# Optimization experiments

Measured on AMD Instinct MI355X. Metric: run time of the kernel, lower is better.

The kernel has to match this reference:

```python
import jax, jax.numpy as jnp
import numpy as np

WIN = (8, 8)
NUM_HEADS = 8
DIM = 256


def _relative_position_index(wh, ww):
    ch = np.arange(wh)
    cw = np.arange(ww)
    coords = np.stack(np.meshgrid(ch, cw, indexing='ij'))  # [2, wh, ww]
    cf = coords.reshape(2, -1)                              # [2, N]
    rel = cf[:, :, None] - cf[:, None, :]                   # [2, N, N]
    rel = rel.transpose(1, 2, 0).copy()
    rel[:, :, 0] += wh - 1
    rel[:, :, 1] += ww - 1
    rel[:, :, 0] *= 2 * ww - 1
    return rel.sum(-1).astype(np.int32)                     # [N, N]


def setup_inputs() -> dict:
    key = jax.random.key(0)
    ks = jax.random.split(key, 7)
    N = WIN[0] * WIN[1]
    BW = 4096  # num_windows * batch
    x = jax.random.normal(ks[0], (BW, N, DIM), dtype=jnp.float32)
    # 0 / -inf style shift mask; random 0 or -100 per entry for generality
    mask = jnp.where(jax.random.uniform(ks[1], (BW, N, N)) < 0.2, -100.0, 0.0).astype(jnp.float32)
    rpb_table = jax.random.normal(ks[2], ((2 * WIN[0] - 1) * (2 * WIN[1] - 1), NUM_HEADS), dtype=jnp.float32) * 0.02
    qkv_w = jax.random.normal(ks[3], (3 * DIM, DIM), dtype=jnp.float32) * (DIM ** -0.5)
    qkv_b = jax.random.normal(ks[4], (3 * DIM,), dtype=jnp.float32) * 0.01
    proj_w = jax.random.normal(ks[5], (DIM, DIM), dtype=jnp.float32) * (DIM ** -0.5)
    proj_b = jax.random.normal(ks[6], (DIM,), dtype=jnp.float32) * 0.01
    rel_idx = jnp.asarray(_relative_position_index(*WIN))
    return {"x": x, "mask": mask, "rpb_table": rpb_table, "qkv_w": qkv_w,
            "qkv_b": qkv_b, "proj_w": proj_w, "proj_b": proj_b, "rel_idx": rel_idx}


def reference(x, mask, rpb_table, qkv_w, qkv_b, proj_w, proj_b, rel_idx):
    B_, N, C = x.shape
    H = NUM_HEADS
    hd = C // H
    scale = hd ** -0.5
    qkv = x @ qkv_w.T + qkv_b                               # [B_, N, 3C]
    qkv = qkv.reshape(B_, N, 3, H, hd).transpose(2, 0, 3, 1, 4)  # [3, B_, H, N, hd]
    q, k, v = qkv[0], qkv[1], qkv[2]
    attn = jnp.einsum('bhnd,bhmd->bhnm', q * scale, k)      # [B_, H, N, N]
    bias = rpb_table[rel_idx.reshape(-1)].reshape(N, N, H).transpose(2, 0, 1)  # [H, N, N]
    attn = attn + bias[None]
    nW = mask.shape[0]
    attn = attn.reshape(B_ // nW, nW, H, N, N) + mask[None, :, None]
    attn = attn.reshape(B_, H, N, N)
    attn = jax.nn.softmax(attn, axis=-1)
    out = jnp.einsum('bhnm,bhmd->bhnd', attn, v)            # [B_, H, N, hd]
    out = out.transpose(0, 2, 1, 3).reshape(B_, N, C)
    return out @ proj_w.T + proj_b
```

## Files before the change

### kernel.cpp

```cpp
#include <hip/hip_runtime.h>

typedef _Float16 half_t;
typedef __attribute__((ext_vector_type(4))) _Float16 half4;
typedef __attribute__((ext_vector_type(8))) _Float16 half8;
typedef __attribute__((ext_vector_type(4))) float f32x4;

#define WS_W1   0
#define WS_W2   (768*256*2)
#define WS_BIAS (WS_W2 + 256*256*2)
#define QK_SCALE 0.17677669529663687f

__global__ __launch_bounds__(256) void prep_kernel(
    const float* __restrict__ qkv_w, const float* __restrict__ proj_w,
    const float* __restrict__ rpb, const int* __restrict__ rel_idx,
    char* __restrict__ ws) {
  int tid = blockIdx.x * 256 + threadIdx.x;
  half_t* W1 = (half_t*)(ws + WS_W1);
  half_t* W2 = (half_t*)(ws + WS_W2);
  float* BIASP = (float*)(ws + WS_BIAS);
  if (tid < 768 * 256) {
    int n = tid >> 8;
    float v = qkv_w[tid];
    if (n < 256) v *= QK_SCALE;
    W1[tid] = (half_t)v;
  }
  if (tid < 256 * 256) W2[tid] = (half_t)proj_w[tid];
  if (tid < 8 * 4096) {
    int r   = tid & 3;
    int l16 = (tid >> 2) & 15;
    int q   = (tid >> 6) & 3;
    int nt  = (tid >> 8) & 3;
    int mt  = (tid >> 10) & 3;
    int h   = (tid >> 12) & 7;
    int i = 16 * mt + l16;
    int j = 16 * nt + 4 * q + r;
    BIASP[tid] = rpb[rel_idx[i * 64 + j] * 8 + h];
  }
}

__device__ __forceinline__ void qkv_gemm(const half_t* Xs, const half_t* W1,
                                         int n0, int l16, int quad,
                                         f32x4 acc[2][4]) {
#pragma unroll
  for (int ks = 0; ks < 8; ++ks) {
    half8 af[4];
#pragma unroll
    for (int mt = 0; mt < 4; ++mt)
      af[mt] = *(const half8*)(&Xs[(16 * mt + l16) * 264 + 32 * ks + quad * 8]);
#pragma unroll
    for (int nt = 0; nt < 2; ++nt) {
      half8 bf = *(const half8*)(&W1[(size_t)(n0 + 16 * nt + l16) * 256 + 32 * ks + quad * 8]);
#pragma unroll
      for (int mt = 0; mt < 4; ++mt)
        acc[nt][mt] = __builtin_amdgcn_mfma_f32_16x16x32_f16(af[mt], bf, acc[nt][mt], 0, 0, 0);
    }
  }
}

__global__ __attribute__((amdgpu_flat_work_group_size(512, 512),
                          amdgpu_waves_per_eu(4, 4))) void fused_kernel(
    const float* __restrict__ x, const float* __restrict__ mask,
    const float* __restrict__ qkv_b, const float* __restrict__ proj_b,
    const char* __restrict__ ws, float* __restrict__ out, int nW) {
  __shared__ __align__(16) half_t Xs[64 * 264];
  __shared__ __align__(16) half_t Ms[64 * 68];
  __shared__ __align__(16) half_t Scr[8][2304];

  const int b = blockIdx.x;
  const int tid = threadIdx.x;
  const int wave = tid >> 6, lane = tid & 63;
  const int l16 = lane & 15, quad = lane >> 4;
  const f32x4 z4 = {0.f, 0.f, 0.f, 0.f};
  const half_t* W1 = (const half_t*)(ws + WS_W1);
  half_t* Sw = &Scr[wave][0];

  {
    const float4* xw = (const float4*)(x + (size_t)b * 16384);
#pragma unroll
    for (int i = 0; i < 8; ++i) {
      int idx4 = tid + i * 512;
      float4 v = xw[idx4];
      int e = idx4 << 2;
      int row = e >> 8, col = e & 255;
      half4 pk;
      pk[0] = (half_t)v.x; pk[1] = (half_t)v.y; pk[2] = (half_t)v.z; pk[3] = (half_t)v.w;
      *(half4*)(&Xs[row * 264 + col]) = pk;
    }
    const float4* mw = (const float4*)(mask + (size_t)(b % nW) * 4096);
#pragma unroll
    for (int i = 0; i < 2; ++i) {
      int idx4 = tid + i * 512;
      float4 v = mw[idx4];
      int e = idx4 << 2;
      int mi = e >> 6, mj = e & 63;
      half4 pk;
      pk[0] = (half_t)v.x; pk[1] = (half_t)v.y; pk[2] = (half_t)v.z; pk[3] = (half_t)v.w;
      *(half4*)(&Ms[mi * 68 + mj]) = pk;
    }
  }
  __syncthreads();

  const int h = wave;
  half4 vh[2][4];
  half8 qf[4];
  half8 kf[4];

  {
    f32x4 acc[2][4];
#pragma unroll
    for (int nt = 0; nt < 2; ++nt)
#pragma unroll
      for (int mt = 0; mt < 4; ++mt) acc[nt][mt] = z4;
    const int n0 = 512 + 32 * h;
    qkv_gemm(Xs, W1, n0, l16, quad, acc);
#pragma unroll
    for (int nt = 0; nt < 2; ++nt) {
      float vb = qkv_b[n0 + 16 * nt + l16];
#pragma unroll
      for (int mt = 0; mt < 4; ++mt)
#pragma unroll
        for (int r = 0; r < 4; ++r)
          vh[nt][mt][r] = (half_t)(acc[nt][mt][r] + vb);
    }
  }

  {
    f32x4 acc[2][4];
#pragma unroll
    for (int nt = 0; nt < 2; ++nt)
#pragma unroll
      for (int mt = 0; mt < 4; ++mt) acc[nt][mt] = z4;
    const int n0 = 32 * h;
    qkv_gemm(Xs, W1, n0, l16, quad, acc);
#pragma unroll
    for (int nt = 0; nt < 2; ++nt) {
      float qb = qkv_b[n0 + 16 * nt + l16] * QK_SCALE;
#pragma unroll
      for (int mt = 0; mt < 4; ++mt)
#pragma unroll
        for (int r = 0; r < 4; ++r)
          Sw[(16 * mt + 4 * quad + r) * 36 + 16 * nt + l16] = (half_t)(acc[nt][mt][r] + qb);
    }
#pragma unroll
    for (int mt = 0; mt < 4; ++mt) {
      union { half8 v; half4 hh[2]; } u;
      u.hh[0] = *(const half4*)(&Sw[(16 * mt + l16) * 36 + quad * 8]);
      u.hh[1] = *(const half4*)(&Sw[(16 * mt + l16) * 36 + quad * 8 + 4]);
      qf[mt] = u.v;
    }
    asm volatile("s_waitcnt lgkmcnt(0)" ::: "memory");
  }

  {
    f32x4 acc[2][4];
#pragma unroll
    for (int nt = 0; nt < 2; ++nt)
#pragma unroll
      for (int mt = 0; mt < 4; ++mt) acc[nt][mt] = z4;
    const int n0 = 256 + 32 * h;
    qkv_gemm(Xs, W1, n0, l16, quad, acc);
#pragma unroll
    for (int nt = 0; nt < 2; ++nt) {
      float kb = qkv_b[n0 + 16 * nt + l16];
#pragma unroll
      for (int mt = 0; mt < 4; ++mt)
#pragma unroll
        for (int r = 0; r < 4; ++r)
          Sw[(16 * mt + 4 * quad + r) * 36 + 16 * nt + l16] = (half_t)(acc[nt][mt][r] + kb);
    }
#pragma unroll
    for (int jt = 0; jt < 4; ++jt) {
      union { half8 v; half4 hh[2]; } u;
      u.hh[0] = *(const half4*)(&Sw[(16 * jt + l16) * 36 + quad * 8]);
      u.hh[1] = *(const half4*)(&Sw[(16 * jt + l16) * 36 + quad * 8 + 4]);
      kf[jt] = u.v;
    }
  }

  half4 oh[4][2];
  {
    const float4* BP4 = (const float4*)(ws + WS_BIAS);
#pragma unroll
    for (int it = 0; it < 4; ++it) {
      f32x4 Sj[4];
#pragma unroll
      for (int jt = 0; jt < 4; ++jt)
        Sj[jt] = __builtin_amdgcn_mfma_f32_16x16x32_f16(kf[jt], qf[it], z4, 0, 0, 0);
#pragma unroll
      for (int jt = 0; jt < 4; ++jt) {
        float4 bv = BP4[(size_t)(((h * 4 + it) * 4 + jt) * 64) + quad * 16 + l16];
        half4 mk = *(const half4*)(&Ms[(16 * it + l16) * 68 + 16 * jt + 4 * quad]);
#pragma unroll
        for (int r = 0; r < 4; ++r)
          Sj[jt][r] += ((const float*)&bv)[r] + (float)mk[r];
      }
      float mx = Sj[0][0];
#pragma unroll
      for (int jt = 0; jt < 4; ++jt)
#pragma unroll
        for (int r = 0; r < 4; ++r) mx = fmaxf(mx, Sj[jt][r]);
      mx = fmaxf(mx, __shfl_xor(mx, 16, 64));
      mx = fmaxf(mx, __shfl_xor(mx, 32, 64));
      float s = 0.f;
      half4 ph[4];
#pragma unroll
      for (int jt = 0; jt < 4; ++jt)
#pragma unroll
        for (int r = 0; r < 4; ++r) {
          float e = exp2f((Sj[jt][r] - mx) * 1.44269504f);
          s += e;
          ph[jt][r] = (half_t)e;
        }
      s += __shfl_xor(s, 16, 64);
      s += __shfl_xor(s, 32, 64);
      float linv = __builtin_amdgcn_rcpf(s);
      f32x4 o0 = z4, o1 = z4;
#pragma unroll
      for (int jt = 0; jt < 4; ++jt) {
        o0 = __builtin_amdgcn_mfma_f32_16x16x16f16(vh[0][jt], ph[jt], o0, 0, 0, 0);
        o1 = __builtin_amdgcn_mfma_f32_16x16x16f16(vh[1][jt], ph[jt], o1, 0, 0, 0);
      }
#pragma unroll
      for (int r = 0; r < 4; ++r) {
        oh[it][0][r] = (half_t)(o0[r] * linv);
        oh[it][1][r] = (half_t)(o1[r] * linv);
      }
    }
  }
  __syncthreads();

#pragma unroll
  for (int it = 0; it < 4; ++it)
#pragma unroll
    for (int dt = 0; dt < 2; ++dt)
      *(half4*)(&Xs[(16 * it + l16) * 264 + 32 * h + 16 * dt + 4 * quad]) = oh[it][dt];
  __syncthreads();

  {
    const half_t* W2 = (const half_t*)(ws + WS_W2);
    const int nb = wave * 32;
    f32x4 C[2][4];
#pragma unroll
    for (int nt = 0; nt < 2; ++nt)
#pragma unroll
      for (int mt = 0; mt < 4; ++mt) C[nt][mt] = z4;
#pragma unroll
    for (int ks = 0; ks < 8; ++ks) {
      half8 af[4];
#pragma unroll
      for (int mt = 0; mt < 4; ++mt)
        af[mt] = *(const half8*)(&Xs[(16 * mt + l16) * 264 + 32 * ks + quad * 8]);
#pragma unroll
      for (int nt = 0; nt < 2; ++nt) {
        half8 bf = *(const half8*)(&W2[(size_t)(nb + 16 * nt + l16) * 256 + 32 * ks + quad * 8]);
#pragma unroll
        for (int mt = 0; mt < 4; ++mt)
          C[nt][mt] = __builtin_amdgcn_mfma_f32_16x16x32_f16(af[mt], bf, C[nt][mt], 0, 0, 0);
      }
    }
#pragma unroll
    for (int nt = 0; nt < 2; ++nt) {
      int c = nb + 16 * nt + l16;
      float pb = proj_b[c];
#pragma unroll
      for (int mt = 0; mt < 4; ++mt)
#pragma unroll
        for (int r = 0; r < 4; ++r) {
          int t = 16 * mt + 4 * quad + r;
          out[(size_t)b * 16384 + t * 256 + c] = C[nt][mt][r] + pb;
        }
    }
  }
}

extern "C" void kernel_launch(void* const* d_in, const int* in_sizes, int n_in,
                              void* d_out, int out_size, void* d_ws, size_t ws_size,
                              hipStream_t stream) {
  const float* x      = (const float*)d_in[0];
  const float* mask   = (const float*)d_in[1];
  const float* rpb    = (const float*)d_in[2];
  const float* qkv_w  = (const float*)d_in[3];
  const float* qkv_b  = (const float*)d_in[4];
  const float* proj_w = (const float*)d_in[5];
  const float* proj_b = (const float*)d_in[6];
  const int*   rel    = (const int*)d_in[7];
  float* out = (float*)d_out;
  char* ws = (char*)d_ws;
  int B_ = in_sizes[0] / 16384;
  int nW = in_sizes[1] / 4096;
  hipLaunchKernelGGL(prep_kernel, dim3(768), dim3(256), 0, stream,
                     qkv_w, proj_w, rpb, rel, ws);
  hipLaunchKernelGGL(fused_kernel, dim3(B_), dim3(512), 0, stream,
                     x, mask, qkv_b, proj_b, (const char*)ws, out, nW);
}
```

Before: 829.2 us.

## Halve block to 4 waves handling two heads each, read mask from global

The fused kernel now launches 256 threads per window instead of 512. Each wave handles two attention heads in sequence and computes 64 output columns in the projection GEMM. The mask is no longer staged in LDS as fp16; it is read directly from global memory as float4 inside the softmax loop, and the scratch area shrinks to four waves. The aim is to cut LDS use so more blocks fit per CU and to drop the mask staging pass. The cost is less parallelism per block, more serial work per wave, higher register pressure from the doubled accumulators, and scattered global mask loads.

```diff
diff --git a/kernel.cpp b/kernel.cpp
--- a/kernel.cpp
+++ b/kernel.cpp
@@ -57,14 +57,13 @@
   }
 }
 
-__global__ __attribute__((amdgpu_flat_work_group_size(512, 512),
-                          amdgpu_waves_per_eu(4, 4))) void fused_kernel(
+__global__ __attribute__((amdgpu_flat_work_group_size(256, 256),
+                          amdgpu_waves_per_eu(3, 3))) void fused_kernel(
     const float* __restrict__ x, const float* __restrict__ mask,
     const float* __restrict__ qkv_b, const float* __restrict__ proj_b,
     const char* __restrict__ ws, float* __restrict__ out, int nW) {
   __shared__ __align__(16) half_t Xs[64 * 264];
-  __shared__ __align__(16) half_t Ms[64 * 68];
-  __shared__ __align__(16) half_t Scr[8][2304];
+  __shared__ __align__(16) half_t Scr[4][2304];
 
   const int b = blockIdx.x;
   const int tid = threadIdx.x;
@@ -77,8 +76,8 @@
   {
     const float4* xw = (const float4*)(x + (size_t)b * 16384);
 #pragma unroll
-    for (int i = 0; i < 8; ++i) {
-      int idx4 = tid + i * 512;
+    for (int i = 0; i < 16; ++i) {
+      int idx4 = tid + i * 256;
       float4 v = xw[idx4];
       int e = idx4 << 2;
       int row = e >> 8, col = e & 255;
@@ -86,100 +85,93 @@
       pk[0] = (half_t)v.x; pk[1] = (half_t)v.y; pk[2] = (half_t)v.z; pk[3] = (half_t)v.w;
       *(half4*)(&Xs[row * 264 + col]) = pk;
     }
-    const float4* mw = (const float4*)(mask + (size_t)(b % nW) * 4096);
-#pragma unroll
-    for (int i = 0; i < 2; ++i) {
-      int idx4 = tid + i * 512;
-      float4 v = mw[idx4];
-      int e = idx4 << 2;
-      int mi = e >> 6, mj = e & 63;
-      half4 pk;
-      pk[0] = (half_t)v.x; pk[1] = (half_t)v.y; pk[2] = (half_t)v.z; pk[3] = (half_t)v.w;
-      *(half4*)(&Ms[mi * 68 + mj]) = pk;
-    }
   }
   __syncthreads();
 
-  const int h = wave;
-  half4 vh[2][4];
-  half8 qf[4];
-  half8 kf[4];
-
-  {
-    f32x4 acc[2][4];
-#pragma unroll
-    for (int nt = 0; nt < 2; ++nt)
-#pragma unroll
-      for (int mt = 0; mt < 4; ++mt) acc[nt][mt] = z4;
-    const int n0 = 512 + 32 * h;
-    qkv_gemm(Xs, W1, n0, l16, quad, acc);
-#pragma unroll
-    for (int nt = 0; nt < 2; ++nt) {
-      float vb = qkv_b[n0 + 16 * nt + l16];
-#pragma unroll
-      for (int mt = 0; mt < 4; ++mt)
-#pragma unroll
-        for (int r = 0; r < 4; ++r)
-          vh[nt][mt][r] = (half_t)(acc[nt][mt][r] + vb);
-    }
-  }
-
-  {
-    f32x4 acc[2][4];
-#pragma unroll
-    for (int nt = 0; nt < 2; ++nt)
-#pragma unroll
-      for (int mt = 0; mt < 4; ++mt) acc[nt][mt] = z4;
-    const int n0 = 32 * h;
-    qkv_gemm(Xs, W1, n0, l16, quad, acc);
-#pragma unroll
-    for (int nt = 0; nt < 2; ++nt) {
-      float qb = qkv_b[n0 + 16 * nt + l16] * QK_SCALE;
-#pragma unroll
-      for (int mt = 0; mt < 4; ++mt)
-#pragma unroll
-        for (int r = 0; r < 4; ++r)
-          Sw[(16 * mt + 4 * quad + r) * 36 + 16 * nt + l16] = (half_t)(acc[nt][mt][r] + qb);
-    }
-#pragma unroll
-    for (int mt = 0; mt < 4; ++mt) {
-      union { half8 v; half4 hh[2]; } u;
-      u.hh[0] = *(const half4*)(&Sw[(16 * mt + l16) * 36 + quad * 8]);
-      u.hh[1] = *(const half4*)(&Sw[(16 * mt + l16) * 36 + quad * 8 + 4]);
-      qf[mt] = u.v;
-    }
-    asm volatile("s_waitcnt lgkmcnt(0)" ::: "memory");
-  }
-
-  {
-    f32x4 acc[2][4];
-#pragma unroll
-    for (int nt = 0; nt < 2; ++nt)
-#pragma unroll
-      for (int mt = 0; mt < 4; ++mt) acc[nt][mt] = z4;
-    const int n0 = 256 + 32 * h;
-    qkv_gemm(Xs, W1, n0, l16, quad, acc);
-#pragma unroll
-    for (int nt = 0; nt < 2; ++nt) {
-      float kb = qkv_b[n0 + 16 * nt + l16];
-#pragma unroll
-      for (int mt = 0; mt < 4; ++mt)
-#pragma unroll
-        for (int r = 0; r < 4; ++r)
-          Sw[(16 * mt + 4 * quad + r) * 36 + 16 * nt + l16] = (half_t)(acc[nt][mt][r] + kb);
-    }
-#pragma unroll
-    for (int jt = 0; jt < 4; ++jt) {
-      union { half8 v; half4 hh[2]; } u;
-      u.hh[0] = *(const half4*)(&Sw[(16 * jt + l16) * 36 + quad * 8]);
-      u.hh[1] = *(const half4*)(&Sw[(16 * jt + l16) * 36 + quad * 8 + 4]);
-      kf[jt] = u.v;
-    }
-  }
-
-  half4 oh[4][2];
-  {
-    const float4* BP4 = (const float4*)(ws + WS_BIAS);
+  const float* Mw = mask + (size_t)(b % nW) * 4096;
+  const float4* BP4 = (const float4*)(ws + WS_BIAS);
+  half4 oh[2][4][2];
+
+#pragma unroll
+  for (int hh = 0; hh < 2; ++hh) {
+    const int h = wave + 4 * hh;
+    half4 vh[2][4];
+    half8 qf[4];
+    half8 kf[4];
+
+    {
+      f32x4 acc[2][4];
+#pragma unroll
+      for (int nt = 0; nt < 2; ++nt)
+#pragma unroll
+        for (int mt = 0; mt < 4; ++mt) acc[nt][mt] = z4;
+      const int n0 = 512 + 32 * h;
+      qkv_gemm(Xs, W1, n0, l16, quad, acc);
+#pragma unroll
+      for (int nt = 0; nt < 2; ++nt) {
+        float vb = qkv_b[n0 + 16 * nt + l16];
+#pragma unroll
+        for (int mt = 0; mt < 4; ++mt)
+#pragma unroll
+          for (int r = 0; r < 4; ++r)
+            vh[nt][mt][r] = (half_t)(acc[nt][mt][r] + vb);
+      }
+    }
+
+    {
+      f32x4 acc[2][4];
+#pragma unroll
+      for (int nt = 0; nt < 2; ++nt)
+#pragma unroll
+        for (int mt = 0; mt < 4; ++mt) acc[nt][mt] = z4;
+      const int n0 = 32 * h;
+      qkv_gemm(Xs, W1, n0, l16, quad, acc);
+#pragma unroll
+      for (int nt = 0; nt < 2; ++nt) {
+        float qb = qkv_b[n0 + 16 * nt + l16] * QK_SCALE;
+#pragma unroll
+        for (int mt = 0; mt < 4; ++mt)
+#pragma unroll
+          for (int r = 0; r < 4; ++r)
+            Sw[(16 * mt + 4 * quad + r) * 36 + 16 * nt + l16] = (half_t)(acc[nt][mt][r] + qb);
+      }
+#pragma unroll
+      for (int mt = 0; mt < 4; ++mt) {
+        union { half8 v; half4 hh2[2]; } u;
+        u.hh2[0] = *(const half4*)(&Sw[(16 * mt + l16) * 36 + quad * 8]);
+        u.hh2[1] = *(const half4*)(&Sw[(16 * mt + l16) * 36 + quad * 8 + 4]);
+        qf[mt] = u.v;
+      }
+      asm volatile("s_waitcnt lgkmcnt(0)" ::: "memory");
+    }
+
+    {
+      f32x4 acc[2][4];
+#pragma unroll
+      for (int nt = 0; nt < 2; ++nt)
+#pragma unroll
+        for (int mt = 0; mt < 4; ++mt) acc[nt][mt] = z4;
+      const int n0 = 256 + 32 * h;
+      qkv_gemm(Xs, W1, n0, l16, quad, acc);
+#pragma unroll
+      for (int nt = 0; nt < 2; ++nt) {
+        float kb = qkv_b[n0 + 16 * nt + l16];
+#pragma unroll
+        for (int mt = 0; mt < 4; ++mt)
+#pragma unroll
+          for (int r = 0; r < 4; ++r)
+            Sw[(16 * mt + 4 * quad + r) * 36 + 16 * nt + l16] = (half_t)(acc[nt][mt][r] + kb);
+      }
+#pragma unroll
+      for (int jt = 0; jt < 4; ++jt) {
+        union { half8 v; half4 hh2[2]; } u;
+        u.hh2[0] = *(const half4*)(&Sw[(16 * jt + l16) * 36 + quad * 8]);
+        u.hh2[1] = *(const half4*)(&Sw[(16 * jt + l16) * 36 + quad * 8 + 4]);
+        kf[jt] = u.v;
+      }
+      asm volatile("s_waitcnt lgkmcnt(0)" ::: "memory");
+    }
+
 #pragma unroll
     for (int it = 0; it < 4; ++it) {
       f32x4 Sj[4];
@@ -189,10 +181,10 @@
 #pragma unroll
       for (int jt = 0; jt < 4; ++jt) {
         float4 bv = BP4[(size_t)(((h * 4 + it) * 4 + jt) * 64) + quad * 16 + l16];
-        half4 mk = *(const half4*)(&Ms[(16 * it + l16) * 68 + 16 * jt + 4 * quad]);
+        float4 mv = *(const float4*)(&Mw[(16 * it + l16) * 64 + 16 * jt + 4 * quad]);
 #pragma unroll
         for (int r = 0; r < 4; ++r)
-          Sj[jt][r] += ((const float*)&bv)[r] + (float)mk[r];
+          Sj[jt][r] += ((const float*)&bv)[r] + ((const float*)&mv)[r];
       }
       float mx = Sj[0][0];
 #pragma unroll
@@ -222,26 +214,29 @@
       }
 #pragma unroll
       for (int r = 0; r < 4; ++r) {
-        oh[it][0][r] = (half_t)(o0[r] * linv);
-        oh[it][1][r] = (half_t)(o1[r] * linv);
+        oh[hh][it][0][r] = (half_t)(o0[r] * linv);
+        oh[hh][it][1][r] = (half_t)(o1[r] * linv);
       }
     }
   }
   __syncthreads();
 
 #pragma unroll
-  for (int it = 0; it < 4; ++it)
-#pragma unroll
-    for (int dt = 0; dt < 2; ++dt)
-      *(half4*)(&Xs[(16 * it + l16) * 264 + 32 * h + 16 * dt + 4 * quad]) = oh[it][dt];
+  for (int hh = 0; hh < 2; ++hh)
+#pragma unroll
+    for (int it = 0; it < 4; ++it)
+#pragma unroll
+      for (int dt = 0; dt < 2; ++dt)
+        *(half4*)(&Xs[(16 * it + l16) * 264 + 32 * (wave + 4 * hh) + 16 * dt + 4 * quad]) =
+            oh[hh][it][dt];
   __syncthreads();
 
   {
     const half_t* W2 = (const half_t*)(ws + WS_W2);
-    const int nb = wave * 32;
-    f32x4 C[2][4];
-#pragma unroll
-    for (int nt = 0; nt < 2; ++nt)
+    const int nb = wave * 64;
+    f32x4 C[4][4];
+#pragma unroll
+    for (int nt = 0; nt < 4; ++nt)
 #pragma unroll
       for (int mt = 0; mt < 4; ++mt) C[nt][mt] = z4;
 #pragma unroll
@@ -251,7 +246,7 @@
       for (int mt = 0; mt < 4; ++mt)
         af[mt] = *(const half8*)(&Xs[(16 * mt + l16) * 264 + 32 * ks + quad * 8]);
 #pragma unroll
-      for (int nt = 0; nt < 2; ++nt) {
+      for (int nt = 0; nt < 4; ++nt) {
         half8 bf = *(const half8*)(&W2[(size_t)(nb + 16 * nt + l16) * 256 + 32 * ks + quad * 8]);
 #pragma unroll
         for (int mt = 0; mt < 4; ++mt)
@@ -259,7 +254,7 @@
       }
     }
 #pragma unroll
-    for (int nt = 0; nt < 2; ++nt) {
+    for (int nt = 0; nt < 4; ++nt) {
       int c = nb + 16 * nt + l16;
       float pb = proj_b[c];
 #pragma unroll
@@ -290,6 +285,6 @@
   int nW = in_sizes[1] / 4096;
   hipLaunchKernelGGL(prep_kernel, dim3(768), dim3(256), 0, stream,
                      qkv_w, proj_w, rpb, rel, ws);
-  hipLaunchKernelGGL(fused_kernel, dim3(B_), dim3(512), 0, stream,
+  hipLaunchKernelGGL(fused_kernel, dim3(B_), dim3(256), 0, stream,
                      x, mask, qkv_b, proj_b, (const char*)ws, out, nW);
 }
```

Result: slower. 939.6 us (+13.3%).
